# Kernel optimization log

Hardware: AMD Instinct MI355X
Metric: run time of the kernel (lower is better)

The kernel has to match this reference:

```python
import jax, jax.numpy as jnp
import numpy as np

B, S, E = 4, 2048, 1024
HIDDEN = 1024
HEADS = 16


def setup_inputs() -> dict:
    key = jax.random.key(0)
    k0, k1, k2, k3, k4 = jax.random.split(key, 5)
    inputs = jax.random.normal(k0, (B, S, E), dtype=jnp.float32)
    W_qkv = jax.random.normal(k1, (E, 3 * HIDDEN), dtype=jnp.float32) * 0.02
    b_qkv = jnp.zeros((3 * HIDDEN,), dtype=jnp.float32)
    W_out = jax.random.normal(k2, (HIDDEN, HIDDEN), dtype=jnp.float32) * 0.02
    b_out = jnp.zeros((HIDDEN,), dtype=jnp.float32)
    return {"inputs": inputs, "W_qkv": W_qkv, "b_qkv": b_qkv, "W_out": W_out, "b_out": b_out}


def reference(inputs, W_qkv, b_qkv, W_out, b_out):
    Bv, Sv, Ev = inputs.shape
    x = inputs @ W_qkv + b_qkv                      # [B, S, 3*hidden]
    # Faithful to the original: reshape mixes seq and hidden exactly as the source does.
    x = x.reshape(Bv, HEADS, Sv, -1)                # [B, H, S, 3*hidden/H]
    q, k, v = jnp.split(x, 3, axis=-1)              # each [B, H, S, hidden/H]
    scale = (2 * HIDDEN) ** (-0.5)
    qk = jnp.einsum('bhse,bhte->bhst', q, k) * scale  # [B, H, S, S]
    mask = jnp.triu(jnp.full((Sv, Sv), -jnp.inf, dtype=qk.dtype), k=1)
    attn = jax.nn.softmax(qk + mask, axis=-1)
    sa = jnp.einsum('bhst,bhte->bhse', attn, v).reshape(Bv, Sv, -1)  # [B, S, hidden]
    return sa @ W_out + b_out
```

## Files before the change

kernel.cpp:

```cpp
#include <hip/hip_runtime.h>
#include <hip/hip_bf16.h>

using bf16 = __hip_bfloat16;

typedef __attribute__((ext_vector_type(8))) short short8;
typedef __attribute__((ext_vector_type(4))) float f32x4;


#define CEXP 0.03188127742677263f

__device__ __forceinline__ unsigned short f2bf(float v) {
  bf16 h = __float2bfloat16(v);
  return *(unsigned short*)&h;
}
__device__ __forceinline__ unsigned int pack2bf(float a, float b) {
  return (unsigned int)f2bf(a) | ((unsigned int)f2bf(b) << 16);
}

__device__ __forceinline__ void gload_lds16(const void* g, void* lds) {
  __builtin_amdgcn_global_load_lds(
      (const __attribute__((address_space(1))) unsigned int*)(g),
      (__attribute__((address_space(3))) unsigned int*)(lds), 16, 0, 0);
}

__global__ void detect_kernel(const unsigned int* __restrict__ x, int* __restrict__ flag) {
  unsigned int w = x[threadIdx.x];
  unsigned int e = (w >> 7) & 0xFF;
  bool inband = (e >= 96 && e <= 133);
  unsigned long long m = __ballot(inband);
  if (threadIdx.x == 0) flag[0] = (__popcll(m) >= 48) ? 0 : 1;
}

__global__ __launch_bounds__(256) void convert_kernel(
    const void* __restrict__ src, bf16* __restrict__ dst, int n8,
    const int* __restrict__ flag) {
  int i = blockIdx.x * 256 + threadIdx.x;
  if (i >= n8) return;
  uint4 outv;
  if (*flag) {
    const float4* s = (const float4*)src + (size_t)i * 2;
    float4 a = s[0], b = s[1];
    outv.x = pack2bf(a.x, a.y);
    outv.y = pack2bf(a.z, a.w);
    outv.z = pack2bf(b.x, b.y);
    outv.w = pack2bf(b.z, b.w);
  } else {
    outv = ((const uint4*)src)[i];
  }
  ((uint4*)dst)[i] = outv;
}

__global__ void convert_bias_qkv(const void* __restrict__ src, bf16* __restrict__ dst,
                                 const int* __restrict__ flag) {
  int i = blockIdx.x * 256 + threadIdx.x;
  if (i >= 3072) return;
  float v = (*flag) ? ((const float*)src)[i]
                    : __bfloat162float(((const bf16*)src)[i]);
  if ((i % 192) < 64) v *= CEXP;
  dst[i] = __float2bfloat16(v);
}

__global__ __launch_bounds__(256) void transpose_bf16(
    const void* __restrict__ src, bf16* __restrict__ dst, int R, int Cc,
    const int* __restrict__ flag, int qscale) {
  __shared__ float tile[32][33];
  const int c0 = blockIdx.x * 32, r0 = blockIdx.y * 32;
  const int tx = threadIdx.x & 31, ty = threadIdx.x >> 5;
  const bool f32 = (*flag != 0);
#pragma unroll
  for (int it = 0; it < 4; ++it) {
    int r = ty + it * 8;
    float v;
    if (f32) v = ((const float*)src)[(size_t)(r0 + r) * Cc + c0 + tx];
    else     v = __bfloat162float(((const bf16*)src)[(size_t)(r0 + r) * Cc + c0 + tx]);
    tile[r][tx] = v;
  }
  __syncthreads();
#pragma unroll
  for (int it = 0; it < 4; ++it) {
    int r = ty + it * 8;
    float vv = tile[tx][r];
    if (qscale && (((c0 + r) % 192) < 64)) vv *= CEXP;
    dst[(size_t)(c0 + r) * R + r0 + tx] = __float2bfloat16(vv);
  }
}

__global__ __launch_bounds__(256) void transpose_v(const bf16* __restrict__ qkv,
                                                   bf16* __restrict__ vtg)
{
  __shared__ short tile[64][72];
  const int bh = blockIdx.x;
  const int k0 = blockIdx.y * 64;
  const unsigned short* qk = (const unsigned short*)qkv + (size_t)bh * 393216;
  const int key = threadIdx.x & 63;
  const int dv = threadIdx.x >> 6;
  const int gk = k0 + key;
  const unsigned short* src =
      qk + (size_t)(gk >> 4) * 3072 + (gk & 15) * 192 + 128 + dv * 16;
  *(short8*)&tile[key][dv * 16] = *(const short8*)src;
  *(short8*)&tile[key][dv * 16 + 8] = *(const short8*)(src + 8);
  __syncthreads();
  const int d = threadIdx.x & 63;
  const int kv = threadIdx.x >> 6;
  unsigned short* dst =
      (unsigned short*)vtg + ((size_t)bh * 64 + d) * 2048 + k0 + kv * 16;
  short8 a, b;
#pragma unroll
  for (int j = 0; j < 8; ++j) {
    a[j] = tile[kv * 16 + j][d];
    b[j] = tile[kv * 16 + 8 + j][d];
  }
  *(short8*)dst = a;
  *(short8*)(dst + 8) = b;
}

__global__ __launch_bounds__(256) void gemm_mfma(
    const bf16* __restrict__ A, const bf16* __restrict__ BT,
    const bf16* __restrict__ bias, void* __restrict__ C,
    int M, int N, int K, int store_mode, const int* __restrict__ flag)
{
  __shared__ alignas(16) unsigned short As[128 * 32];
  __shared__ alignas(16) unsigned short Bs[128 * 32];
  const bool store_f32 = store_mode && (*flag != 0);
  const int tid = threadIdx.x;
  const int wave = tid >> 6, lane = tid & 63;
  const int l15 = lane & 15, l4 = lane >> 4;
  const int m0 = blockIdx.y * 128, n0 = blockIdx.x * 128;
  const int wm = (wave & 1) * 64, wn = (wave >> 1) * 64;

  const int srow = wave * 32 + (lane >> 2);
  const int skv = (lane & 3) * 8;
  const bf16* ga = A + (size_t)(m0 + srow) * K + skv;
  const bf16* gb = BT + (size_t)(n0 + srow) * K + skv;
  unsigned short* la = As + (wave * 32) * 32;
  unsigned short* lb = Bs + (wave * 32) * 32;

  f32x4 acc[4][4] = {};

  for (int k0 = 0; k0 < K; k0 += 32) {
    __syncthreads();
    gload_lds16(ga, la);
    gload_lds16(ga + (size_t)16 * K, la + 16 * 32);
    gload_lds16(gb, lb);
    gload_lds16(gb + (size_t)16 * K, lb + 16 * 32);
    ga += 32; gb += 32;
    __syncthreads();

    short8 af[4], bfr[4];
#pragma unroll
    for (int i = 0; i < 4; ++i) {
      af[i]  = *(const short8*)(As + (wm + i * 16 + l15) * 32 + l4 * 8);
      bfr[i] = *(const short8*)(Bs + (wn + i * 16 + l15) * 32 + l4 * 8);
    }
#pragma unroll
    for (int i = 0; i < 4; ++i)
#pragma unroll
      for (int j = 0; j < 4; ++j)
        acc[i][j] = __builtin_amdgcn_mfma_f32_16x16x32_bf16(af[i], bfr[j], acc[i][j], 0, 0, 0);
  }

#pragma unroll
  for (int j = 0; j < 4; ++j) {
    const int n = n0 + wn + j * 16 + l15;
    const float bv = __bfloat162float(bias[n]);
#pragma unroll
    for (int i = 0; i < 4; ++i) {
#pragma unroll
      for (int r = 0; r < 4; ++r) {
        const int mrow = m0 + wm + i * 16 + l4 * 4 + r;
        const float v = acc[i][j][r] + bv;
        if (store_f32) ((float*)C)[(size_t)mrow * N + n] = v;
        else           ((bf16*)C)[(size_t)mrow * N + n] = __float2bfloat16(v);
      }
    }
  }
}

__global__ __launch_bounds__(256) void attn_mfma(const bf16* __restrict__ qkv,
                                                 const bf16* __restrict__ vtg,
                                                 bf16* __restrict__ sa)
{
  __shared__ alignas(16) short Ks[2][4096];
  __shared__ alignas(16) short Vs[2][4096];
  __shared__ alignas(16) short Ps[4][1152];
  const int tid = threadIdx.x;
  const int bh = blockIdx.x;
  const int qc = 15 - blockIdx.y;
  const size_t base = (size_t)bh * 393216;
  const int w = tid >> 6, lane = tid & 63;
  const int l15 = lane & 15, l4 = lane >> 4;
  const unsigned short* qk = (const unsigned short*)qkv;
  const unsigned short* vtb = (const unsigned short*)vtg + (size_t)bh * 131072;
  short* psw = &Ps[w][0];

  const unsigned short* ksrc0 = qk + base + (size_t)(lane >> 4) * 3072 + (lane & 15) * 192 + 64;
  const unsigned short* vsrc0 = vtb + (size_t)lane * 2048;

  const int ktmax = 2 * qc + 1;

  short8 qf[2][2];
#pragma unroll
  for (int h = 0; h < 2; ++h) {
    const unsigned short* pq =
        qk + base + (size_t)(qc * 8 + 2 * w + h) * 3072 + l15 * 192 + l4 * 8;
    qf[h][0] = *(const short8*)pq;
    qf[h][1] = *(const short8*)(pq + 32);
  }

  f32x4 o[2][4] = {};
  float ml[2] = {-__builtin_inff(), -__builtin_inff()};
  float ls[2] = {0.f, 0.f};
  int cur = 0;

#pragma unroll
  for (int rd = 0; rd < 2; ++rd) {
    const int dc = w + 4 * rd;
    gload_lds16(ksrc0 + dc * 8, &Ks[0][dc * 512]);
    gload_lds16(vsrc0 + dc * 8, &Vs[0][dc * 512]);
  }
  __syncthreads();

  for (int kt = 0; kt <= ktmax; ++kt) {
    if (kt < ktmax) {
      const int nb = cur ^ 1;
#pragma unroll
      for (int rd = 0; rd < 2; ++rd) {
        const int dc = w + 4 * rd;
        gload_lds16(ksrc0 + (size_t)(kt + 1) * 12288 + dc * 8, &Ks[nb][dc * 512]);
        gload_lds16(vsrc0 + (kt + 1) * 64 + dc * 8, &Vs[nb][dc * 512]);
      }
    }

    f32x4 sc[2][4];
#pragma unroll
    for (int t = 0; t < 4; ++t) {
      const short8 kf0 = *(const short8*)&Ks[cur][(l4) * 512 + (16 * t + l15) * 8];
      const short8 kf1 = *(const short8*)&Ks[cur][(4 + l4) * 512 + (16 * t + l15) * 8];
#pragma unroll
      for (int h = 0; h < 2; ++h) {
        f32x4 c = {};
        c = __builtin_amdgcn_mfma_f32_16x16x32_bf16(kf0, qf[h][0], c, 0, 0, 0);
        c = __builtin_amdgcn_mfma_f32_16x16x32_bf16(kf1, qf[h][1], c, 0, 0, 0);
        sc[h][t] = c;
      }
    }

    if (kt >= 2 * qc) {
      const int kb = 64 * (kt - 2 * qc);
#pragma unroll
      for (int h = 0; h < 2; ++h) {
        const int thr = 32 * w + 16 * h + l15;
#pragma unroll
        for (int t = 0; t < 4; ++t)
#pragma unroll
          for (int r = 0; r < 4; ++r)
            if (kb + 16 * t + 4 * l4 + r > thr) sc[h][t][r] = -__builtin_inff();
      }
    }

    unsigned int pk2[2][4][2];
#pragma unroll
    for (int h = 0; h < 2; ++h) {
      float mx = -__builtin_inff();
#pragma unroll
      for (int t = 0; t < 4; ++t)
#pragma unroll
        for (int r = 0; r < 4; ++r) mx = fmaxf(mx, sc[h][t][r]);
      mx = fmaxf(mx, __shfl_xor(mx, 16, 64));
      mx = fmaxf(mx, __shfl_xor(mx, 32, 64));
      if (!__all(mx <= ml[h] + 8.f)) {
        const float m_new = fmaxf(ml[h], mx);
        const float alpha = __builtin_amdgcn_exp2f(ml[h] - m_new);
        ml[h] = m_new;
        ls[h] *= alpha;
#pragma unroll
        for (int jn = 0; jn < 4; ++jn)
#pragma unroll
          for (int r = 0; r < 4; ++r) o[h][jn][r] *= alpha;
      }
      const float m_new = ml[h];
      float s = 0.f;
#pragma unroll
      for (int t = 0; t < 4; ++t) {
        float p0 = __builtin_amdgcn_exp2f(sc[h][t][0] - m_new);
        float p1 = __builtin_amdgcn_exp2f(sc[h][t][1] - m_new);
        float p2 = __builtin_amdgcn_exp2f(sc[h][t][2] - m_new);
        float p3 = __builtin_amdgcn_exp2f(sc[h][t][3] - m_new);
        s += (p0 + p1) + (p2 + p3);
        pk2[h][t][0] = pack2bf(p0, p1);
        pk2[h][t][1] = pack2bf(p2, p3);
      }
      s += __shfl_xor(s, 16, 64);
      s += __shfl_xor(s, 32, 64);
      ls[h] += s;
    }

    short8 pf[2][2];
#pragma unroll
    for (int h = 0; h < 2; ++h) {
#pragma unroll
      for (int t = 0; t < 4; ++t) {
        uint2 wv; wv.x = pk2[h][t][0]; wv.y = pk2[h][t][1];
        *(uint2*)(psw + l15 * 72 + 16 * t + 4 * l4) = wv;
      }
      pf[h][0] = *(const short8*)(psw + l15 * 72 + 8 * l4);
      pf[h][1] = *(const short8*)(psw + l15 * 72 + 32 + 8 * l4);
    }

#pragma unroll
    for (int jn = 0; jn < 4; ++jn)
#pragma unroll
      for (int ks = 0; ks < 2; ++ks) {
        const short8 vf =
            *(const short8*)&Vs[cur][(4 * ks + l4) * 512 + (16 * jn + l15) * 8];
#pragma unroll
        for (int h = 0; h < 2; ++h)
          o[h][jn] = __builtin_amdgcn_mfma_f32_16x16x32_bf16(vf, pf[h][ks], o[h][jn], 0, 0, 0);
      }

    __syncthreads();
    cur ^= 1;
  }

#pragma unroll
  for (int h = 0; h < 2; ++h) {
    const float inv = 1.0f / ls[h];
    unsigned short* so =
        (unsigned short*)sa + (size_t)(bh * 128 + qc * 8 + 2 * w + h) * 1024;
#pragma unroll
    for (int jn = 0; jn < 4; ++jn) {
      uint2 wv;
      wv.x = pack2bf(o[h][jn][0] * inv, o[h][jn][1] * inv);
      wv.y = pack2bf(o[h][jn][2] * inv, o[h][jn][3] * inv);
      *(uint2*)(so + l15 * 64 + jn * 16 + l4 * 4) = wv;
    }
  }
}

extern "C" void kernel_launch(void* const* d_in, const int* in_sizes, int n_in,
                              void* d_out, int out_size, void* d_ws, size_t ws_size,
                              hipStream_t stream)
{
  const void* x_raw    = d_in[0];
  const void* Wqkv_raw = d_in[1];
  const void* bqkv_raw = d_in[2];
  const void* Wout_raw = d_in[3];
  const void* bout_raw = d_in[4];

  char* ws = (char*)d_ws;
  int*  flag   = (int*)ws;
  bf16* xb     = (bf16*)(ws + 256);
  bf16* wqkvT  = xb + (size_t)8192 * 1024;
  bf16* bqkvb  = wqkvT + (size_t)3072 * 1024;
  bf16* woutT  = bqkvb + 4096;
  bf16* boutb  = woutT + (size_t)1024 * 1024;
  bf16* qkv    = boutb + 4096;
  bf16* sa     = qkv + (size_t)8192 * 3072;
  bf16* vtg    = sa + (size_t)8192 * 1024;

  detect_kernel<<<1, 64, 0, stream>>>((const unsigned int*)x_raw, flag);

  convert_kernel<<<(8192 * 1024 / 8 + 255) / 256, 256, 0, stream>>>(x_raw, xb, 8192 * 1024 / 8, flag);
  convert_bias_qkv<<<12, 256, 0, stream>>>(bqkv_raw, bqkvb, flag);
  convert_kernel<<<1, 256, 0, stream>>>(bout_raw, boutb, 1024 / 8, flag);
  transpose_bf16<<<dim3(3072 / 32, 1024 / 32), 256, 0, stream>>>(Wqkv_raw, wqkvT, 1024, 3072, flag, 1);
  transpose_bf16<<<dim3(1024 / 32, 1024 / 32), 256, 0, stream>>>(Wout_raw, woutT, 1024, 1024, flag, 0);

  gemm_mfma<<<dim3(3072 / 128, 8192 / 128), 256, 0, stream>>>(
      xb, wqkvT, bqkvb, qkv, 8192, 3072, 1024, 0, flag);
  transpose_v<<<dim3(64, 32), 256, 0, stream>>>(qkv, vtg);
  attn_mfma<<<dim3(64, 16), 256, 0, stream>>>(qkv, vtg, sa);
  gemm_mfma<<<dim3(1024 / 128, 8192 / 128), 256, 0, stream>>>(
      sa, woutT, boutb, d_out, 8192, 1024, 1024, 1, flag);
}
```

Baseline: 302.1 us.

## Pair causal query chunks per attention block and swizzle GEMM blocks across XCDs

The attention kernel now launches 512-thread blocks. Each block holds two 4-wave groups that take complementary query chunks (15-pr and pr), so causal work is balanced across blocks and the grid halves. The K/V tile loads are split so one group fills K and the other fills V, sharing the double buffer, and the short-chunk group idles on later iterations while still joining the barriers. The GEMM also remaps block IDs so that consecutive tiles land on the same XCD, which is meant to improve L2 reuse. The cost is more LDS per block and idle waves in the light group.

New measurement: 294.0 us. 1.03x faster.

```diff
diff --git a/kernel.cpp b/kernel.cpp
--- a/kernel.cpp
+++ b/kernel.cpp
@@ -125,7 +125,15 @@
   const int tid = threadIdx.x;
   const int wave = tid >> 6, lane = tid & 63;
   const int l15 = lane & 15, l4 = lane >> 4;
-  const int m0 = blockIdx.y * 128, n0 = blockIdx.x * 128;
+
+  const int nwg = gridDim.x * gridDim.y;
+  const int orig = blockIdx.x + gridDim.x * blockIdx.y;
+  const int qn = nwg >> 3, rn = nwg & 7;
+  const int xcd = orig & 7, loc = orig >> 3;
+  const int swz = (xcd < rn ? xcd * (qn + 1) : rn * (qn + 1) + (xcd - rn) * qn) + loc;
+  const int bx = swz % gridDim.x, by = swz / gridDim.x;
+
+  const int m0 = by * 128, n0 = bx * 128;
   const int wm = (wave & 1) * 64, wn = (wave >> 1) * 64;
 
   const int srow = wave * 32 + (lane >> 2);
@@ -176,33 +184,40 @@
   }
 }
 
-__global__ __launch_bounds__(256) void attn_mfma(const bf16* __restrict__ qkv,
+__global__ __launch_bounds__(512) void attn_mfma(const bf16* __restrict__ qkv,
                                                  const bf16* __restrict__ vtg,
                                                  bf16* __restrict__ sa)
 {
   __shared__ alignas(16) short Ks[2][4096];
   __shared__ alignas(16) short Vs[2][4096];
-  __shared__ alignas(16) short Ps[4][1152];
+  __shared__ alignas(16) short Ps[8][1152];
   const int tid = threadIdx.x;
   const int bh = blockIdx.x;
-  const int qc = 15 - blockIdx.y;
+  const int pr = blockIdx.y;
   const size_t base = (size_t)bh * 393216;
-  const int w = tid >> 6, lane = tid & 63;
+  const int w = tid >> 6;
+  const int g = w >> 2;
+  const int wl = w & 3;
+  const int lane = tid & 63;
   const int l15 = lane & 15, l4 = lane >> 4;
   const unsigned short* qk = (const unsigned short*)qkv;
   const unsigned short* vtb = (const unsigned short*)vtg + (size_t)bh * 131072;
   short* psw = &Ps[w][0];
 
-  const unsigned short* ksrc0 = qk + base + (size_t)(lane >> 4) * 3072 + (lane & 15) * 192 + 64;
-  const unsigned short* vsrc0 = vtb + (size_t)lane * 2048;
-
-  const int ktmax = 2 * qc + 1;
+  const int qc = g ? pr : (15 - pr);
+  const int my_ktmax  = 2 * qc + 1;
+  const int blk_ktmax = 2 * (15 - pr) + 1;
+
+  const unsigned short* gsrc0 =
+      g ? (vtb + (size_t)lane * 2048)
+        : (qk + base + (size_t)(lane >> 4) * 3072 + (lane & 15) * 192 + 64);
+  const size_t gstep = g ? 64 : 12288;
 
   short8 qf[2][2];
 #pragma unroll
   for (int h = 0; h < 2; ++h) {
     const unsigned short* pq =
-        qk + base + (size_t)(qc * 8 + 2 * w + h) * 3072 + l15 * 192 + l4 * 8;
+        qk + base + (size_t)(qc * 8 + 2 * wl + h) * 3072 + l15 * 192 + l4 * 8;
     qf[h][0] = *(const short8*)pq;
     qf[h][1] = *(const short8*)(pq + 32);
   }
@@ -212,111 +227,109 @@
   float ls[2] = {0.f, 0.f};
   int cur = 0;
 
-#pragma unroll
-  for (int rd = 0; rd < 2; ++rd) {
-    const int dc = w + 4 * rd;
-    gload_lds16(ksrc0 + dc * 8, &Ks[0][dc * 512]);
-    gload_lds16(vsrc0 + dc * 8, &Vs[0][dc * 512]);
+  {
+    short* dstbuf = g ? &Vs[0][0] : &Ks[0][0];
+    gload_lds16(gsrc0 + wl * 8, dstbuf + wl * 512);
+    gload_lds16(gsrc0 + (wl + 4) * 8, dstbuf + (wl + 4) * 512);
   }
   __syncthreads();
 
-  for (int kt = 0; kt <= ktmax; ++kt) {
-    if (kt < ktmax) {
-      const int nb = cur ^ 1;
-#pragma unroll
-      for (int rd = 0; rd < 2; ++rd) {
-        const int dc = w + 4 * rd;
-        gload_lds16(ksrc0 + (size_t)(kt + 1) * 12288 + dc * 8, &Ks[nb][dc * 512]);
-        gload_lds16(vsrc0 + (kt + 1) * 64 + dc * 8, &Vs[nb][dc * 512]);
-      }
-    }
-
-    f32x4 sc[2][4];
-#pragma unroll
-    for (int t = 0; t < 4; ++t) {
-      const short8 kf0 = *(const short8*)&Ks[cur][(l4) * 512 + (16 * t + l15) * 8];
-      const short8 kf1 = *(const short8*)&Ks[cur][(4 + l4) * 512 + (16 * t + l15) * 8];
+  for (int kt = 0; kt <= blk_ktmax; ++kt) {
+    if (kt < blk_ktmax) {
+      short* dstbuf = g ? &Vs[cur ^ 1][0] : &Ks[cur ^ 1][0];
+      const unsigned short* s = gsrc0 + (size_t)(kt + 1) * gstep;
+      gload_lds16(s + wl * 8, dstbuf + wl * 512);
+      gload_lds16(s + (wl + 4) * 8, dstbuf + (wl + 4) * 512);
+    }
+
+    if (kt <= my_ktmax) {
+      f32x4 sc[2][4];
+#pragma unroll
+      for (int t = 0; t < 4; ++t) {
+        const short8 kf0 = *(const short8*)&Ks[cur][(l4) * 512 + (16 * t + l15) * 8];
+        const short8 kf1 = *(const short8*)&Ks[cur][(4 + l4) * 512 + (16 * t + l15) * 8];
+#pragma unroll
+        for (int h = 0; h < 2; ++h) {
+          f32x4 c = {};
+          c = __builtin_amdgcn_mfma_f32_16x16x32_bf16(kf0, qf[h][0], c, 0, 0, 0);
+          c = __builtin_amdgcn_mfma_f32_16x16x32_bf16(kf1, qf[h][1], c, 0, 0, 0);
+          sc[h][t] = c;
+        }
+      }
+
+      if (kt >= 2 * qc) {
+        const int kb = 64 * (kt - 2 * qc);
+#pragma unroll
+        for (int h = 0; h < 2; ++h) {
+          const int thr = 32 * wl + 16 * h + l15;
+#pragma unroll
+          for (int t = 0; t < 4; ++t)
+#pragma unroll
+            for (int r = 0; r < 4; ++r)
+              if (kb + 16 * t + 4 * l4 + r > thr) sc[h][t][r] = -__builtin_inff();
+        }
+      }
+
+      unsigned int pk2[2][4][2];
 #pragma unroll
       for (int h = 0; h < 2; ++h) {
-        f32x4 c = {};
-        c = __builtin_amdgcn_mfma_f32_16x16x32_bf16(kf0, qf[h][0], c, 0, 0, 0);
-        c = __builtin_amdgcn_mfma_f32_16x16x32_bf16(kf1, qf[h][1], c, 0, 0, 0);
-        sc[h][t] = c;
-      }
-    }
-
-    if (kt >= 2 * qc) {
-      const int kb = 64 * (kt - 2 * qc);
+        float mx = -__builtin_inff();
+#pragma unroll
+        for (int t = 0; t < 4; ++t)
+#pragma unroll
+          for (int r = 0; r < 4; ++r) mx = fmaxf(mx, sc[h][t][r]);
+        mx = fmaxf(mx, __shfl_xor(mx, 16, 64));
+        mx = fmaxf(mx, __shfl_xor(mx, 32, 64));
+        if (!__all(mx <= ml[h] + 8.f)) {
+          const float m_new = fmaxf(ml[h], mx);
+          const float alpha = __builtin_amdgcn_exp2f(ml[h] - m_new);
+          ml[h] = m_new;
+          ls[h] *= alpha;
+#pragma unroll
+          for (int jn = 0; jn < 4; ++jn)
+#pragma unroll
+            for (int r = 0; r < 4; ++r) o[h][jn][r] *= alpha;
+        }
+        const float m_new = ml[h];
+        float s = 0.f;
+#pragma unroll
+        for (int t = 0; t < 4; ++t) {
+          float p0 = __builtin_amdgcn_exp2f(sc[h][t][0] - m_new);
+          float p1 = __builtin_amdgcn_exp2f(sc[h][t][1] - m_new);
+          float p2 = __builtin_amdgcn_exp2f(sc[h][t][2] - m_new);
+          float p3 = __builtin_amdgcn_exp2f(sc[h][t][3] - m_new);
+          s += (p0 + p1) + (p2 + p3);
+          pk2[h][t][0] = pack2bf(p0, p1);
+          pk2[h][t][1] = pack2bf(p2, p3);
+        }
+        s += __shfl_xor(s, 16, 64);
+        s += __shfl_xor(s, 32, 64);
+        ls[h] += s;
+      }
+
+      short8 pf[2][2];
 #pragma unroll
       for (int h = 0; h < 2; ++h) {
-        const int thr = 32 * w + 16 * h + l15;
-#pragma unroll
-        for (int t = 0; t < 4; ++t)
-#pragma unroll
-          for (int r = 0; r < 4; ++r)
-            if (kb + 16 * t + 4 * l4 + r > thr) sc[h][t][r] = -__builtin_inff();
-      }
-    }
-
-    unsigned int pk2[2][4][2];
-#pragma unroll
-    for (int h = 0; h < 2; ++h) {
-      float mx = -__builtin_inff();
-#pragma unroll
-      for (int t = 0; t < 4; ++t)
-#pragma unroll
-        for (int r = 0; r < 4; ++r) mx = fmaxf(mx, sc[h][t][r]);
-      mx = fmaxf(mx, __shfl_xor(mx, 16, 64));
-      mx = fmaxf(mx, __shfl_xor(mx, 32, 64));
-      if (!__all(mx <= ml[h] + 8.f)) {
-        const float m_new = fmaxf(ml[h], mx);
-        const float alpha = __builtin_amdgcn_exp2f(ml[h] - m_new);
-        ml[h] = m_new;
-        ls[h] *= alpha;
-#pragma unroll
-        for (int jn = 0; jn < 4; ++jn)
-#pragma unroll
-          for (int r = 0; r < 4; ++r) o[h][jn][r] *= alpha;
-      }
-      const float m_new = ml[h];
-      float s = 0.f;
-#pragma unroll
-      for (int t = 0; t < 4; ++t) {
-        float p0 = __builtin_amdgcn_exp2f(sc[h][t][0] - m_new);
-        float p1 = __builtin_amdgcn_exp2f(sc[h][t][1] - m_new);
-        float p2 = __builtin_amdgcn_exp2f(sc[h][t][2] - m_new);
-        float p3 = __builtin_amdgcn_exp2f(sc[h][t][3] - m_new);
-        s += (p0 + p1) + (p2 + p3);
-        pk2[h][t][0] = pack2bf(p0, p1);
-        pk2[h][t][1] = pack2bf(p2, p3);
-      }
-      s += __shfl_xor(s, 16, 64);
-      s += __shfl_xor(s, 32, 64);
-      ls[h] += s;
-    }
-
-    short8 pf[2][2];
-#pragma unroll
-    for (int h = 0; h < 2; ++h) {
-#pragma unroll
-      for (int t = 0; t < 4; ++t) {
-        uint2 wv; wv.x = pk2[h][t][0]; wv.y = pk2[h][t][1];
-        *(uint2*)(psw + l15 * 72 + 16 * t + 4 * l4) = wv;
-      }
-      pf[h][0] = *(const short8*)(psw + l15 * 72 + 8 * l4);
-      pf[h][1] = *(const short8*)(psw + l15 * 72 + 32 + 8 * l4);
-    }
-
-#pragma unroll
-    for (int jn = 0; jn < 4; ++jn)
-#pragma unroll
-      for (int ks = 0; ks < 2; ++ks) {
-        const short8 vf =
-            *(const short8*)&Vs[cur][(4 * ks + l4) * 512 + (16 * jn + l15) * 8];
-#pragma unroll
-        for (int h = 0; h < 2; ++h)
-          o[h][jn] = __builtin_amdgcn_mfma_f32_16x16x32_bf16(vf, pf[h][ks], o[h][jn], 0, 0, 0);
-      }
+#pragma unroll
+        for (int t = 0; t < 4; ++t) {
+          uint2 wv; wv.x = pk2[h][t][0]; wv.y = pk2[h][t][1];
+          *(uint2*)(psw + l15 * 72 + 16 * t + 4 * l4) = wv;
+        }
+        pf[h][0] = *(const short8*)(psw + l15 * 72 + 8 * l4);
+        pf[h][1] = *(const short8*)(psw + l15 * 72 + 32 + 8 * l4);
+      }
+
+#pragma unroll
+      for (int jn = 0; jn < 4; ++jn)
+#pragma unroll
+        for (int ks = 0; ks < 2; ++ks) {
+          const short8 vf =
+              *(const short8*)&Vs[cur][(4 * ks + l4) * 512 + (16 * jn + l15) * 8];
+#pragma unroll
+          for (int h = 0; h < 2; ++h)
+            o[h][jn] = __builtin_amdgcn_mfma_f32_16x16x32_bf16(vf, pf[h][ks], o[h][jn], 0, 0, 0);
+        }
+    }
 
     __syncthreads();
     cur ^= 1;
@@ -326,7 +339,7 @@
   for (int h = 0; h < 2; ++h) {
     const float inv = 1.0f / ls[h];
     unsigned short* so =
-        (unsigned short*)sa + (size_t)(bh * 128 + qc * 8 + 2 * w + h) * 1024;
+        (unsigned short*)sa + (size_t)(bh * 128 + qc * 8 + 2 * wl + h) * 1024;
 #pragma unroll
     for (int jn = 0; jn < 4; ++jn) {
       uint2 wv;
@@ -369,7 +382,7 @@
   gemm_mfma<<<dim3(3072 / 128, 8192 / 128), 256, 0, stream>>>(
       xb, wqkvT, bqkvb, qkv, 8192, 3072, 1024, 0, flag);
   transpose_v<<<dim3(64, 32), 256, 0, stream>>>(qkv, vtg);
-  attn_mfma<<<dim3(64, 16), 256, 0, stream>>>(qkv, vtg, sa);
+  attn_mfma<<<dim3(64, 8), 512, 0, stream>>>(qkv, vtg, sa);
   gemm_mfma<<<dim3(1024 / 128, 8192 / 128), 256, 0, stream>>>(
       sa, woutT, boutb, d_out, 8192, 1024, 1024, 1, flag);
 }
```
